# Kernel tuning notes

Hardware: AMD Instinct MI355X
Metric: run time of the kernel (lower is better)

## Reference

```python
import jax, jax.numpy as jnp
import numpy as np

B, L, D = 16, 512, 128   # batch of sequences, seq len, input_dim
BN_EPS = 1e-5
TEMP = 1.0


def setup_inputs() -> dict:
    key = jax.random.key(0)
    ks = jax.random.split(key, 5)
    ids = jax.random.randint(ks[0], (B, L), 0, 50000)            # item ids per (seq, pos)
    log_mask = jnp.ones((B, L), dtype=jnp.int32)                 # all positions valid (static N)
    x1 = jax.random.normal(ks[1], (B * L, D), dtype=jnp.float32)
    x2 = jax.random.normal(ks[2], (B * L, D), dtype=jnp.float32)
    w1 = jax.random.normal(ks[3], (2 * D, D), dtype=jnp.float32) * 0.05  # torch Linear: [out, in]
    b1 = jnp.zeros((2 * D,), jnp.float32)
    w2 = jax.random.normal(ks[4], (D, 2 * D), dtype=jnp.float32) * 0.05
    b2 = jnp.zeros((D,), jnp.float32)
    gamma = jnp.ones((D,), jnp.float32)   # BatchNorm1d affine weight
    beta = jnp.zeros((D,), jnp.float32)   # BatchNorm1d affine bias
    return dict(ids=ids, log_mask=log_mask, x1=x1, x2=x2,
                w1=w1, b1=b1, w2=w2, b2=b2, gamma=gamma, beta=beta)


def _embed(x, w1, b1, w2, b2, gamma, beta):
    """linear1 -> relu -> linear2 -> BatchNorm1d (train-mode batch stats) -> L2 normalize."""
    h = jax.nn.relu(x @ w1.T + b1)
    y = h @ w2.T + b2
    mu = y.mean(axis=0)
    var = ((y - mu) ** 2).mean(axis=0)          # biased var, as torch BN uses for normalization
    y = (y - mu) * jax.lax.rsqrt(var + BN_EPS) * gamma + beta
    return y / jnp.linalg.norm(y, axis=1, keepdims=True)


def reference(ids, log_mask, x1, x2, w1, b1, w2, b2, gamma, beta):
    # log_mask is all-nonzero in this setup, so the gather by nonzero indices is the identity.
    nb, nl = ids.shape
    N = x1.shape[0]                      # = nb * nl valid anchors
    ids_f = ids.reshape(-1)
    seq = jnp.repeat(jnp.arange(nb), nl)  # seq_indexs: which sequence each row belongs to

    z1 = _embed(x1, w1, b1, w2, b2, gamma, beta)
    z2 = _embed(x2, w1, b1, w2, b2, gamma, beta)
    S = z1 @ z2.T                        # [N, N] cosine similarity (rows already unit-norm)

    idx = jnp.arange(N)
    ids_next = jnp.roll(ids_f, -1)
    seq_next = jnp.roll(seq, -1)
    # two-positive branch: i < N-1 and same sequence as the next row
    two = (idx < N - 1) & (seq == seq_next)            # [N] bool

    diag = jnp.diagonal(S)                             # cos(anchor_i, input2_i)
    s_next = S[idx, (idx + 1) % N]                     # cos(anchor_i, input2_{i+1})

    cols = idx[None, :]
    neg1 = ids_f[None, :] != ids_f[:, None]                                # single-pos negatives
    neg2 = neg1 & (ids_f[None, :] != ids_next[:, None]) & (seq[None, :] != seq[:, None])
    mask = jnp.where(two[:, None], neg2, neg1)
    # add the positives (self, and i+1 in the two-positive branch)
    mask = mask | (cols == idx[:, None]) | (two[:, None] & (cols == idx[:, None] + 1))

    denom = jnp.sum(jnp.where(mask, jnp.exp(S / TEMP), 0.0), axis=1)       # [N]
    pos_sum = diag + jnp.where(two, s_next, 0.0)
    n_pos = 1.0 + two.astype(S.dtype)

    inner = -(pos_sum / TEMP - jnp.log(denom)) / n_pos
    return jnp.sum(inner) / N
```

## Files before the change

kernel.cpp:

```cpp
#include <hip/hip_runtime.h>

#define N_TOT 8192
#define SEQ_L 512
#define D 128
#define NCHUNK 16
#define CHUNK (N_TOT / NCHUNK)
#define NJT_H 4
#define NDIAG 272
#define LOG2E 1.4426950408889634f
#define LN2   0.6931471805599453f

using bf16x8  = __attribute__((ext_vector_type(8))) short;
using f32x4   = __attribute__((ext_vector_type(4))) float;

static __device__ __forceinline__ unsigned short f2bf(float f) {
    unsigned int u = __float_as_uint(f);
    u = (u + 0x7FFFu + ((u >> 16) & 1u)) >> 16;
    return (unsigned short)u;
}
static __device__ __forceinline__ float bf2f(unsigned short h) {
    return __uint_as_float(((unsigned int)h) << 16);
}
static __device__ __forceinline__ float dot8(bf16x8 a, bf16x8 b) {
    float s = 0.f;
    #pragma unroll
    for (int k = 0; k < 8; ++k)
        s = fmaf(bf2f((unsigned short)a[k]), bf2f((unsigned short)b[k]), s);
    return s;
}

__global__ __launch_bounds__(256) void convert_w_kernel(
    const float* __restrict__ w1, const float* __restrict__ w2,
    unsigned short* __restrict__ w1b, unsigned short* __restrict__ w2b)
{
    int idx = blockIdx.x * 256 + threadIdx.x;
    const float* src = (idx < 8192) ? w1 : w2;
    unsigned short* dst = (idx < 8192) ? w1b : w2b;
    int off = ((idx < 8192) ? idx : idx - 8192) * 4;
    float4 v = *(const float4*)(src + off);
    ushort4 o;
    o.x = f2bf(v.x); o.y = f2bf(v.y); o.z = f2bf(v.z); o.w = f2bf(v.w);
    *(ushort4*)(dst + off) = o;
}

__global__ __launch_bounds__(256) void mlp_mfma_kernel(
    const float* __restrict__ x1, const float* __restrict__ x2,
    const unsigned short* __restrict__ w1b, const float* __restrict__ b1,
    const unsigned short* __restrict__ w2b, const float* __restrict__ b2,
    unsigned short* __restrict__ z1, unsigned short* __restrict__ z2,
    float* __restrict__ part_s, float* __restrict__ part_ss)
{
    __shared__ unsigned short hsh[32][264];
    const int t = threadIdx.x;
    const int w = t >> 6;
    const int lane = t & 63;
    const int g = lane >> 4;
    const int c16 = lane & 15;
    const int tensor = blockIdx.x >> 8;
    const int blk = blockIdx.x & 255;
    const int r0 = blk * 32;
    const float* __restrict__ x = tensor ? x2 : x1;
    unsigned short* __restrict__ z = tensor ? z2 : z1;

    bf16x8 af[2][4];
    #pragma unroll
    for (int rf = 0; rf < 2; ++rf)
        #pragma unroll
        for (int ks = 0; ks < 4; ++ks) {
            const float* xp = x + (size_t)(r0 + rf * 16 + c16) * D + ks * 32 + g * 8;
            float4 u0 = *(const float4*)xp;
            float4 u1 = *(const float4*)(xp + 4);
            bf16x8 a;
            a[0] = f2bf(u0.x); a[1] = f2bf(u0.y); a[2] = f2bf(u0.z); a[3] = f2bf(u0.w);
            a[4] = f2bf(u1.x); a[5] = f2bf(u1.y); a[6] = f2bf(u1.z); a[7] = f2bf(u1.w);
            af[rf][ks] = a;
        }
    f32x4 acc1[2][4] = {};
    #pragma unroll
    for (int ks = 0; ks < 4; ++ks)
        #pragma unroll
        for (int nf = 0; nf < 4; ++nf) {
            int n = w * 64 + nf * 16 + c16;
            bf16x8 b = *(const bf16x8*)(w1b + (size_t)n * D + ks * 32 + g * 8);
            #pragma unroll
            for (int rf = 0; rf < 2; ++rf)
                acc1[rf][nf] = __builtin_amdgcn_mfma_f32_16x16x32_bf16(af[rf][ks], b, acc1[rf][nf], 0, 0, 0);
        }
    #pragma unroll
    for (int nf = 0; nf < 4; ++nf) {
        float bb = b1[w * 64 + nf * 16 + c16];
        #pragma unroll
        for (int rf = 0; rf < 2; ++rf)
            #pragma unroll
            for (int r = 0; r < 4; ++r)
                hsh[rf * 16 + g * 4 + r][w * 64 + nf * 16 + c16] = f2bf(fmaxf(acc1[rf][nf][r] + bb, 0.f));
    }
    __syncthreads();

    f32x4 acc2[2][2] = {};
    #pragma unroll
    for (int ks = 0; ks < 8; ++ks) {
        bf16x8 a0 = *(const bf16x8*)(&hsh[c16][ks * 32 + g * 8]);
        bf16x8 a1 = *(const bf16x8*)(&hsh[16 + c16][ks * 32 + g * 8]);
        #pragma unroll
        for (int nf = 0; nf < 2; ++nf) {
            int n = w * 32 + nf * 16 + c16;
            bf16x8 b = *(const bf16x8*)(w2b + (size_t)n * 256 + ks * 32 + g * 8);
            acc2[0][nf] = __builtin_amdgcn_mfma_f32_16x16x32_bf16(a0, b, acc2[0][nf], 0, 0, 0);
            acc2[1][nf] = __builtin_amdgcn_mfma_f32_16x16x32_bf16(a1, b, acc2[1][nf], 0, 0, 0);
        }
    }

    #pragma unroll
    for (int nf = 0; nf < 2; ++nf) {
        int col = w * 32 + nf * 16 + c16;
        float bb = b2[col];
        float s = 0.f, ss = 0.f;
        #pragma unroll
        for (int rf = 0; rf < 2; ++rf)
            #pragma unroll
            for (int r = 0; r < 4; ++r) {
                float v = acc2[rf][nf][r] + bb;
                z[(size_t)(r0 + rf * 16 + g * 4 + r) * D + col] = f2bf(v);
                s += v; ss += v * v;
            }
        s  += __shfl_xor(s, 16);  s  += __shfl_xor(s, 32);
        ss += __shfl_xor(ss, 16); ss += __shfl_xor(ss, 32);
        if (g == 0) {
            part_s [((size_t)tensor * 256 + blk) * D + col] = s;
            part_ss[((size_t)tensor * 256 + blk) * D + col] = ss;
        }
    }
}

__global__ __launch_bounds__(256) void bn_reduce_kernel(
    const float* __restrict__ part_s, const float* __restrict__ part_ss,
    const float* __restrict__ gamma,
    float* __restrict__ mu, float* __restrict__ sc)
{
    const int t = threadIdx.x;
    const int tensor = blockIdx.x >> 7;
    const int col = blockIdx.x & 127;
    float s  = part_s [((size_t)tensor * 256 + t) * D + col];
    float ss = part_ss[((size_t)tensor * 256 + t) * D + col];
    #pragma unroll
    for (int m = 32; m; m >>= 1) { s += __shfl_xor(s, m); ss += __shfl_xor(ss, m); }
    __shared__ float rs[4], rss[4];
    if ((t & 63) == 0) { rs[t >> 6] = s; rss[t >> 6] = ss; }
    __syncthreads();
    if (t == 0) {
        float S = rs[0] + rs[1] + rs[2] + rs[3];
        float SS = rss[0] + rss[1] + rss[2] + rss[3];
        float m = S / (float)N_TOT;
        float var = SS / (float)N_TOT - m * m;
        mu[tensor * D + col] = m;
        sc[tensor * D + col] = gamma[col] * rsqrtf(var + 1e-5f);
    }
}

__global__ __launch_bounds__(256) void bn_l2_kernel(
    unsigned short* __restrict__ z1, unsigned short* __restrict__ z2,
    const float* __restrict__ mu, const float* __restrict__ sc,
    const float* __restrict__ beta)
{
    const int t = threadIdx.x;
    const int wv = t >> 6;
    const int lane = t & 63;
    const int rw = lane >> 5;
    const int cl = lane & 31;
    const int grow = blockIdx.x * 8 + wv * 2 + rw;
    const int tensor = grow >> 13;
    const int row = grow & (N_TOT - 1);

    unsigned short* __restrict__ yr = (tensor ? z2 : z1) + (size_t)row * D + cl * 4;
    float4 m4 = *(const float4*)(mu + tensor * D + cl * 4);
    float4 s4 = *(const float4*)(sc + tensor * D + cl * 4);
    float4 b4 = *(const float4*)(beta + cl * 4);
    ushort4 v = *(const ushort4*)yr;
    float v0 = (bf2f(v.x) - m4.x) * s4.x + b4.x;
    float v1 = (bf2f(v.y) - m4.y) * s4.y + b4.y;
    float v2 = (bf2f(v.z) - m4.z) * s4.z + b4.z;
    float v3 = (bf2f(v.w) - m4.w) * s4.w + b4.w;
    float ssq = v0 * v0 + v1 * v1 + v2 * v2 + v3 * v3;
    #pragma unroll
    for (int m = 16; m; m >>= 1) ssq += __shfl_xor(ssq, m);
    float rn = rsqrtf(ssq);
    if (tensor == 0) rn *= LOG2E;
    ushort4 o;
    o.x = f2bf(v0 * rn); o.y = f2bf(v1 * rn);
    o.z = f2bf(v2 * rn); o.w = f2bf(v3 * rn);
    *(ushort4*)yr = o;
}

__global__ __launch_bounds__(256, 2) void loss_all_kernel(
    const short* __restrict__ z1, const short* __restrict__ z2,
    const int* __restrict__ ids,
    float* __restrict__ posv, float* __restrict__ dden,
    float* __restrict__ den_part)
{
    const int t = threadIdx.x;
    const int bid = blockIdx.x;

    if (bid < 256) {
        const int row = bid * 32 + (t >> 3);
        const int le = t & 7;
        const short* ap = z1 + (size_t)row * D + le * 16;
        const short* bp = z2 + (size_t)row * D + le * 16;
        const short* cp = z2 + (size_t)((row + 1) & (N_TOT - 1)) * D + le * 16;
        bf16x8 a0 = *(const bf16x8*)ap, a1 = *(const bf16x8*)(ap + 8);
        float s1 = dot8(a0, *(const bf16x8*)bp) + dot8(a1, *(const bf16x8*)(bp + 8));
        float s2 = dot8(a0, *(const bf16x8*)cp) + dot8(a1, *(const bf16x8*)(cp + 8));
        #pragma unroll
        for (int m = 1; m < 8; m <<= 1) { s1 += __shfl_xor(s1, m); s2 += __shfl_xor(s2, m); }
        if (le == 0) {
            bool two = (row & (SEQ_L - 1)) != (SEQ_L - 1);
            if (two) {
                posv[row] = (s1 + s2) * LN2;
                dden[row] = exp2f(s1) + exp2f(s2);
            } else {
                posv[row] = s1 * LN2;
            }
        }
        return;
    }
    if (bid < NDIAG) {
        __shared__ float red[4];
        const int sr = bid - 256;
        const int i = sr * SEQ_L + (SEQ_L - 1);
        const int jbase = sr * SEQ_L;
        const int idi_ = ids[i];
        float acc = 0.f;
        #pragma unroll
        for (int c = 0; c < 2; ++c) {
            int j = jbase + t * 2 + c;
            float s = 0.f;
            for (int k = 0; k < 16; ++k) {
                bf16x8 va = *(const bf16x8*)(z1 + (size_t)i * D + k * 8);
                bf16x8 vb = *(const bf16x8*)(z2 + (size_t)j * D + k * 8);
                s += dot8(va, vb);
            }
            bool m = (ids[j] != idi_) | (j == i);
            acc += m ? exp2f(s) : 0.f;
        }
        #pragma unroll
        for (int m = 32; m; m >>= 1) acc += __shfl_xor(acc, m);
        if ((t & 63) == 0) red[t >> 6] = acc;
        __syncthreads();
        if (t == 0) dden[i] = red[0] + red[1] + red[2] + red[3];
        return;
    }

    const int bidm = bid - NDIAG;
    const int w    = t >> 6;
    const int lane = t & 63;
    const int g    = lane >> 4;
    const int c16  = lane & 15;

    const int c15  = bidm % 15;
    const int rbh  = bidm / 15;
    const int rbi  = rbh >> 1;
    const int half = rbh & 1;
    const int rb   = rbi * 256;
    const int seqb = rb >> 9;
    const int chunk = c15 + (c15 >= seqb);
    const int jbase = chunk * CHUNK + half * 256;

    const int i_wb = rb + w * 64;

    __shared__ __align__(16) unsigned char z2s[2][64 * 256];

    const int srow = t >> 2;
    const int sq   = t & 3;
    const int wxor = (srow & 7) << 4;
    const int rxor = (c16 & 7) << 4;

    bf16x8 af[4][4];
    #pragma unroll
    for (int rf = 0; rf < 4; ++rf)
        #pragma unroll
        for (int ks = 0; ks < 4; ++ks)
            af[rf][ks] = *(const bf16x8*)(z1 + (size_t)(i_wb + rf * 16 + c16) * D + ks * 32 + g * 8);

    int idi[4][4], idn_s[4][4];
    #pragma unroll
    for (int rf = 0; rf < 4; ++rf)
        #pragma unroll
        for (int r = 0; r < 4; ++r) {
            int i = i_wb + rf * 16 + g * 4 + r;
            idi[rf][r] = ids[i];
            bool tw = ((i & (SEQ_L - 1)) != (SEQ_L - 1));
            idn_s[rf][r] = tw ? ids[(i + 1) & (N_TOT - 1)] : idi[rf][r];
        }

    #pragma unroll
    for (int it = 0; it < 4; ++it) {
        bf16x8 v = *(const bf16x8*)(z2 + (size_t)(jbase + srow) * D + sq * 8 + it * 32);
        *(bf16x8*)&z2s[0][srow * 256 + ((sq * 16 + it * 64) ^ wxor)] = v;
    }
    __syncthreads();

    float den[4][4] = {};
    int cbuf = 0;

    #pragma unroll 1
    for (int jt = 0; jt < NJT_H; ++jt) {
        const int cb = jbase + jt * 64;

        bf16x8 stg[4];
        if (jt + 1 < NJT_H) {
            #pragma unroll
            for (int it = 0; it < 4; ++it)
                stg[it] = *(const bf16x8*)(z2 + (size_t)(cb + 64 + srow) * D + sq * 8 + it * 32);
        }

        int idj[4];
        #pragma unroll
        for (int nf = 0; nf < 4; ++nf) idj[nf] = ids[cb + nf * 16 + c16];

        f32x4 acc[4][4] = {};
        #pragma unroll
        for (int ks = 0; ks < 4; ++ks)
            #pragma unroll
            for (int nf = 0; nf < 4; ++nf) {
                bf16x8 b = *(const bf16x8*)&z2s[cbuf][(nf * 16 + c16) * 256 + ((ks * 64 + g * 16) ^ rxor)];
                #pragma unroll
                for (int rf = 0; rf < 4; ++rf)
                    acc[rf][nf] = __builtin_amdgcn_mfma_f32_16x16x32_bf16(af[rf][ks], b, acc[rf][nf], 0, 0, 0);
            }

        if (jt + 1 < NJT_H) {
            #pragma unroll
            for (int it = 0; it < 4; ++it)
                *(bf16x8*)&z2s[cbuf ^ 1][srow * 256 + ((sq * 16 + it * 64) ^ wxor)] = stg[it];
        }
        __syncthreads();

        #pragma unroll
        for (int rf = 0; rf < 4; ++rf)
            #pragma unroll
            for (int nf = 0; nf < 4; ++nf)
                #pragma unroll
                for (int r = 0; r < 4; ++r) {
                    float e = exp2f(acc[rf][nf][r]);
                    bool m = (idj[nf] != idi[rf][r]) & (idj[nf] != idn_s[rf][r]);
                    den[rf][r] += m ? e : 0.f;
                }
        cbuf ^= 1;
    }

    #pragma unroll
    for (int rf = 0; rf < 4; ++rf)
        #pragma unroll
        for (int r = 0; r < 4; ++r) {
            float dsum = den[rf][r];
            dsum += __shfl_xor(dsum, 1);
            dsum += __shfl_xor(dsum, 2);
            dsum += __shfl_xor(dsum, 4);
            dsum += __shfl_xor(dsum, 8);
            if (c16 == 0)
                den_part[(chunk * 2 + half) * N_TOT + i_wb + rf * 16 + g * 4 + r] = dsum;
        }
}

__global__ __launch_bounds__(256) void loss_finish1_kernel(
    const float* __restrict__ den_part, const float* __restrict__ posv,
    const float* __restrict__ dden, float* __restrict__ partial)
{
    const int t = threadIdx.x;
    const int row = blockIdx.x * 256 + t;
    const int seqb = row >> 9;
    float den = dden[row];
    #pragma unroll
    for (int q = 0; q < 2 * NCHUNK; ++q)
        if ((q >> 1) != seqb) den += den_part[q * N_TOT + row];
    bool two = ((row & (SEQ_L - 1)) != (SEQ_L - 1));
    float npos = two ? 2.f : 1.f;
    float v = -(posv[row] - logf(den)) / npos;

    #pragma unroll
    for (int m = 32; m; m >>= 1) v += __shfl_xor(v, m);
    __shared__ float red[4];
    if ((t & 63) == 0) red[t >> 6] = v;
    __syncthreads();
    if (t == 0) partial[blockIdx.x] = red[0] + red[1] + red[2] + red[3];
}

__global__ __launch_bounds__(64) void loss_finish2_kernel(
    const float* __restrict__ partial, float* __restrict__ out)
{
    const int t = threadIdx.x;
    float v = (t < 32) ? partial[t] : 0.f;
    #pragma unroll
    for (int m = 32; m; m >>= 1) v += __shfl_xor(v, m);
    if (t == 0) out[0] = v / (float)N_TOT;
}

extern "C" void kernel_launch(void* const* d_in, const int* in_sizes, int n_in,
                              void* d_out, int out_size, void* d_ws, size_t ws_size,
                              hipStream_t stream)
{
    const int*   ids   = (const int*)d_in[0];
    const float* x1    = (const float*)d_in[2];
    const float* x2    = (const float*)d_in[3];
    const float* w1    = (const float*)d_in[4];
    const float* b1    = (const float*)d_in[5];
    const float* w2    = (const float*)d_in[6];
    const float* b2    = (const float*)d_in[7];
    const float* gamma = (const float*)d_in[8];
    const float* beta  = (const float*)d_in[9];

    char* ws = (char*)d_ws;
    unsigned short* z1b = (unsigned short*)ws;
    unsigned short* z2b = (unsigned short*)(ws + (2u << 20));
    float* part_s  = (float*)(ws + (4u << 20));
    float* part_ss = part_s + 2 * 256 * D;
    float* mu      = part_ss + 2 * 256 * D;
    float* sc      = mu + 2 * D;
    float* den_part = sc + 2 * D;
    float* posv    = den_part + 2 * NCHUNK * N_TOT;
    float* dden    = posv + N_TOT;
    float* partial = dden + N_TOT;
    unsigned short* w1b = (unsigned short*)(partial + 64);
    unsigned short* w2b = w1b + 256 * D;

    convert_w_kernel<<<64, 256, 0, stream>>>(w1, w2, w1b, w2b);
    mlp_mfma_kernel<<<512, 256, 0, stream>>>(x1, x2, w1b, b1, w2b, b2,
                                             z1b, z2b, part_s, part_ss);
    bn_reduce_kernel<<<256, 256, 0, stream>>>(part_s, part_ss, gamma, mu, sc);
    bn_l2_kernel<<<2048, 256, 0, stream>>>(z1b, z2b, mu, sc, beta);
    loss_all_kernel<<<NDIAG + 960, 256, 0, stream>>>((const short*)z1b, (const short*)z2b,
                                                     ids, posv, dden, den_part);
    loss_finish1_kernel<<<32, 256, 0, stream>>>(den_part, posv, dden, partial);
    loss_finish2_kernel<<<1, 64, 0, stream>>>(partial, (float*)d_out);
}
```

Measured before the change: 86.89 us.

## Deepen z2 tile prefetch to two stages and stage column ids in LDS

The similarity-tile loop now prefetches z2 tiles two iterations ahead into registers and is fully unrolled. Column ids for the block's 256 columns are loaded once into shared memory instead of being read from global memory on every tile. The __syncthreads is replaced by an explicit lgkmcnt wait, a sched_barrier and s_barrier, so outstanding global loads no longer have to drain at each barrier. The goal is to hide global load latency behind the MFMA work, at the cost of more registers for the second staging buffer and the unrolled loop.

```diff
diff --git a/kernel.cpp b/kernel.cpp
--- a/kernel.cpp
+++ b/kernel.cpp
@@ -28,6 +28,12 @@
         s = fmaf(bf2f((unsigned short)a[k]), bf2f((unsigned short)b[k]), s);
     return s;
 }
+
+#define PIPE_BARRIER() do {                                        \
+    asm volatile("s_waitcnt lgkmcnt(0)" ::: "memory");             \
+    __builtin_amdgcn_sched_barrier(0);                             \
+    __builtin_amdgcn_s_barrier();                                  \
+} while (0)
 
 __global__ __launch_bounds__(256) void convert_w_kernel(
     const float* __restrict__ w1, const float* __restrict__ w2,
@@ -227,12 +233,12 @@
         __shared__ float red[4];
         const int sr = bid - 256;
         const int i = sr * SEQ_L + (SEQ_L - 1);
-        const int jbase = sr * SEQ_L;
+        const int jbase0 = sr * SEQ_L;
         const int idi_ = ids[i];
         float acc = 0.f;
         #pragma unroll
         for (int c = 0; c < 2; ++c) {
-            int j = jbase + t * 2 + c;
+            int j = jbase0 + t * 2 + c;
             float s = 0.f;
             for (int k = 0; k < 16; ++k) {
                 bf16x8 va = *(const bf16x8*)(z1 + (size_t)i * D + k * 8);
@@ -268,11 +274,14 @@
     const int i_wb = rb + w * 64;
 
     __shared__ __align__(16) unsigned char z2s[2][64 * 256];
+    __shared__ int ids_sh[256];
 
     const int srow = t >> 2;
     const int sq   = t & 3;
     const int wxor = (srow & 7) << 4;
     const int rxor = (c16 & 7) << 4;
+
+    int my_idj = ids[jbase + t];
 
     bf16x8 af[4][4];
     #pragma unroll
@@ -292,37 +301,39 @@
             idn_s[rf][r] = tw ? ids[(i + 1) & (N_TOT - 1)] : idi[rf][r];
         }
 
-    #pragma unroll
-    for (int it = 0; it < 4; ++it) {
-        bf16x8 v = *(const bf16x8*)(z2 + (size_t)(jbase + srow) * D + sq * 8 + it * 32);
-        *(bf16x8*)&z2s[0][srow * 256 + ((sq * 16 + it * 64) ^ wxor)] = v;
-    }
-    __syncthreads();
+    bf16x8 stg[2][4];
+    #pragma unroll
+    for (int b = 0; b < 2; ++b)
+        #pragma unroll
+        for (int it = 0; it < 4; ++it)
+            stg[b][it] = *(const bf16x8*)(z2 + (size_t)(jbase + b * 64 + srow) * D + sq * 8 + it * 32);
+
+    ids_sh[t] = my_idj;
+    #pragma unroll
+    for (int it = 0; it < 4; ++it)
+        *(bf16x8*)&z2s[0][srow * 256 + ((sq * 16 + it * 64) ^ wxor)] = stg[0][it];
+    PIPE_BARRIER();
 
     float den[4][4] = {};
-    int cbuf = 0;
-
-    #pragma unroll 1
+
+    #pragma unroll
     for (int jt = 0; jt < NJT_H; ++jt) {
-        const int cb = jbase + jt * 64;
-
-        bf16x8 stg[4];
-        if (jt + 1 < NJT_H) {
+        if (jt + 2 < NJT_H) {
             #pragma unroll
             for (int it = 0; it < 4; ++it)
-                stg[it] = *(const bf16x8*)(z2 + (size_t)(cb + 64 + srow) * D + sq * 8 + it * 32);
+                stg[jt & 1][it] = *(const bf16x8*)(z2 + (size_t)(jbase + (jt + 2) * 64 + srow) * D + sq * 8 + it * 32);
         }
 
         int idj[4];
         #pragma unroll
-        for (int nf = 0; nf < 4; ++nf) idj[nf] = ids[cb + nf * 16 + c16];
+        for (int nf = 0; nf < 4; ++nf) idj[nf] = ids_sh[jt * 64 + nf * 16 + c16];
 
         f32x4 acc[4][4] = {};
         #pragma unroll
         for (int ks = 0; ks < 4; ++ks)
             #pragma unroll
             for (int nf = 0; nf < 4; ++nf) {
-                bf16x8 b = *(const bf16x8*)&z2s[cbuf][(nf * 16 + c16) * 256 + ((ks * 64 + g * 16) ^ rxor)];
+                bf16x8 b = *(const bf16x8*)&z2s[jt & 1][(nf * 16 + c16) * 256 + ((ks * 64 + g * 16) ^ rxor)];
                 #pragma unroll
                 for (int rf = 0; rf < 4; ++rf)
                     acc[rf][nf] = __builtin_amdgcn_mfma_f32_16x16x32_bf16(af[rf][ks], b, acc[rf][nf], 0, 0, 0);
@@ -331,9 +342,9 @@
         if (jt + 1 < NJT_H) {
             #pragma unroll
             for (int it = 0; it < 4; ++it)
-                *(bf16x8*)&z2s[cbuf ^ 1][srow * 256 + ((sq * 16 + it * 64) ^ wxor)] = stg[it];
-        }
-        __syncthreads();
+                *(bf16x8*)&z2s[(jt + 1) & 1][srow * 256 + ((sq * 16 + it * 64) ^ wxor)] = stg[(jt + 1) & 1][it];
+            PIPE_BARRIER();
+        }
 
         #pragma unroll
         for (int rf = 0; rf < 4; ++rf)
@@ -345,7 +356,6 @@
                     bool m = (idj[nf] != idi[rf][r]) & (idj[nf] != idn_s[rf][r]);
                     den[rf][r] += m ? e : 0.f;
                 }
-        cbuf ^= 1;
     }
 
     #pragma unroll
```

After: 120.6 us. 1.39x slower.
